# Kernel tuning notes

Measured on AMD Instinct MI355X. Metric: run time of the kernel, lower is better.

## Reference

```python
import jax, jax.numpy as jnp
import numpy as np

P, F_IN, HG, C, T, E, HOUT = 4096, 64, 64, 64, 32, 65536, 12
LEAKY_SLOPE = 0.2
LN_EPS = 1e-5


def setup_inputs() -> dict:
    key = jax.random.key(0)
    ks = jax.random.split(key, 14)
    g = lambda k, shape, scale: (jax.random.normal(k, shape, jnp.float32) * scale)
    return {
        "X": jax.random.normal(ks[0], (1, P, F_IN, T), jnp.float32),
        "edge_index": jax.random.randint(ks[1], (T, 2, E), 0, P, jnp.int32),
        # GATv2 params (single head)
        "Wl": g(ks[2], (F_IN, HG), 0.1),
        "Wr": g(ks[3], (F_IN, HG), 0.1),
        "att": g(ks[4], (HG,), 0.1),
        "gat_b": g(ks[5], (HG,), 0.02),
        # 1x1 time conv (HG -> C) and 1x1 residual conv (F_IN -> C)
        "W_time": g(ks[6], (C, HG), 0.1),
        "b_time": g(ks[7], (C,), 0.02),
        "W_res": g(ks[8], (C, F_IN), 0.1),
        "b_res": g(ks[9], (C,), 0.02),
        # LayerNorm over channel dim C
        "ln_g": jnp.ones((C,), jnp.float32),
        "ln_b": jnp.zeros((C,), jnp.float32),
        # final conv: Conv2d(in=T, out=HOUT, kernel=(1, C)) -> weight (HOUT, T, C)
        "W_final": g(ks[10], (HOUT, T, C), 0.05),
        "b_final": g(ks[11], (HOUT,), 0.02),
    }


def reference(X, edge_index, Wl, Wr, att, gat_b, W_time, b_time, W_res, b_res,
              ln_g, ln_b, W_final, b_final):
    Pn = X.shape[1]

    def gat_t(x, edges):
        # x: (P, F_IN), edges: (2, E) with edges[0]=src j, edges[1]=dst i
        src, dst = edges[0], edges[1]
        hl = x @ Wl                      # (P, HG) messages
        hr = x @ Wr                      # (P, HG) query side
        e = jax.nn.leaky_relu(hl[src] + hr[dst], LEAKY_SLOPE) @ att  # (E,)
        emax = jax.ops.segment_max(e, dst, num_segments=Pn)
        ex = jnp.exp(e - emax[dst])
        den = jax.ops.segment_sum(ex, dst, num_segments=Pn)
        alpha = ex / den[dst]            # softmax over in-edges of each dst
        return jax.ops.segment_sum(alpha[:, None] * hl[src], dst,
                                   num_segments=Pn) + gat_b  # (P, HG)

    xs = jnp.moveaxis(X[0], -1, 0)                     # (T, P, F_IN)
    X_hat = jax.nn.relu(jax.vmap(gat_t)(xs, edge_index))  # (T, P, HG)

    th = jnp.einsum('tph,ch->tpc', X_hat, W_time) + b_time  # time conv 1x1
    rs = jnp.einsum('tpf,cf->tpc', xs, W_res) + b_res       # residual conv 1x1
    y = jax.nn.relu(th + rs)                                 # (T, P, C)

    mu = jnp.mean(y, axis=-1, keepdims=True)
    var = jnp.var(y, axis=-1, keepdims=True)
    yn = (y - mu) * jax.lax.rsqrt(var + LN_EPS) * ln_g + ln_b  # (T, P, C)

    # final conv: in-channels = T, kernel (1, C) -> contract over t and c
    out = jnp.einsum('tpc,otc->po', yn, W_final) + b_final     # (P, HOUT)
    return out[None]                                           # (1, P, HOUT)
```

## Files before the change

kernel.cpp:

```cpp
#include <hip/hip_runtime.h>
#include <math.h>

#define NP 4096
#define F_IN 64
#define HG 64
#define NC 64
#define NT 32
#define NE 65536
#define HOUT 12
#define LEAKY 0.2f
#define LN_EPS 1e-5f

template <int CTRL>
__device__ __forceinline__ float dppadd(float v, float x) {
    int r = __builtin_amdgcn_update_dpp(0, __builtin_bit_cast(int, x), CTRL, 0xF, 0xF, false);
    return v + __builtin_bit_cast(float, r);
}
__device__ __forceinline__ float rowsum16(float v) {
    v = dppadd<0x128>(v, v);
    v = dppadd<0x124>(v, v);
    v = dppadd<0x122>(v, v);
    v = dppadd<0x121>(v, v);
    return v;
}
__device__ __forceinline__ float laneXorSum(float v) {
    v += __shfl_xor(v, 16, 64);
    v += __shfl_xor(v, 32, 64);
    return v;
}
__device__ __forceinline__ int waveSumInt(int v) {
#pragma unroll
    for (int d = 1; d < 64; d <<= 1) v += __shfl_xor(v, d, 64);
    return v;
}

#define FMA4(Acomp, B, r)                                                     \
    acc[r][0] += (Acomp) * (B).x; acc[r][1] += (Acomp) * (B).y;               \
    acc[r][2] += (Acomp) * (B).z; acc[r][3] += (Acomp) * (B).w;

__global__ __launch_bounds__(256) void k_prep(const float* __restrict__ W_time,
        const float* __restrict__ W_res, const float* __restrict__ bf,
        float* __restrict__ wtT, float* __restrict__ wrT, float* __restrict__ out) {
    int b = blockIdx.x, tid = threadIdx.x;
    if (b < 16) {
        int i = b * 256 + tid;
        wtT[i] = W_time[(i & 63) * 64 + (i >> 6)];
    } else if (b < 32) {
        int i = (b - 16) * 256 + tid;
        wrT[i] = W_res[(i & 63) * 64 + (i >> 6)];
    } else {
        int i = (b - 32) * 256 + tid;
        out[i] = bf[i % HOUT];
    }
}

__global__ __launch_bounds__(256) void k_hlhr(const float* __restrict__ X,
        const float* __restrict__ Wl, const float* __restrict__ Wr,
        const float* __restrict__ wrT, const float* __restrict__ b_res,
        float* __restrict__ hl, float* __restrict__ hr, float* __restrict__ rs) {
    __shared__ float xs[2][F_IN][36];
    __shared__ float bk[F_IN][132];
    int p0 = blockIdx.x * 2, tid = threadIdx.x;
    const float4* Xp = (const float4*)(X + (size_t)p0 * F_IN * NT);
    for (int i4 = tid; i4 < 1024; i4 += 256) {
        int pp = i4 >> 9, f = (i4 >> 3) & 63, t0 = (i4 & 7) * 4;
        *(float4*)&xs[pp][f][t0] = Xp[i4];
    }
    const float4* Wl4 = (const float4*)Wl;
    const float4* Wr4 = (const float4*)Wr;
    for (int i4 = tid; i4 < 1024; i4 += 256) {
        int f = i4 >> 4, h4 = (i4 & 15) * 4;
        *(float4*)&bk[f][h4] = Wl4[i4];
        *(float4*)&bk[f][64 + h4] = Wr4[i4];
    }
    __syncthreads();
    {
        int ng = tid & 31, tg = tid >> 5;
        int n0 = ng * 4, col = (ng & 15) * 4, t0 = tg * 4;
        float acc[8][4];
#pragma unroll
        for (int i = 0; i < 8; ++i)
#pragma unroll
            for (int j = 0; j < 4; ++j) acc[i][j] = 0.f;
#pragma unroll 4
        for (int f = 0; f < F_IN; ++f) {
            float4 B = *(const float4*)&bk[f][n0];
            float4 A0 = *(const float4*)&xs[0][f][t0];
            float4 A1 = *(const float4*)&xs[1][f][t0];
            FMA4(A0.x, B, 0) FMA4(A0.y, B, 1) FMA4(A0.z, B, 2) FMA4(A0.w, B, 3)
            FMA4(A1.x, B, 4) FMA4(A1.y, B, 5) FMA4(A1.z, B, 6) FMA4(A1.w, B, 7)
        }
#pragma unroll
        for (int pp = 0; pp < 2; ++pp) {
#pragma unroll
            for (int i = 0; i < 4; ++i) {
                size_t rb = ((size_t)(t0 + i) * NP + p0 + pp) * HG;
                float4 v;
                v.x = acc[pp * 4 + i][0]; v.y = acc[pp * 4 + i][1];
                v.z = acc[pp * 4 + i][2]; v.w = acc[pp * 4 + i][3];
                if (ng < 16) *(float4*)&hl[rb + col] = v;
                else         *(float4*)&hr[rb + col] = v;
            }
        }
    }
    __syncthreads();
    {
        const float4* wrT4 = (const float4*)wrT;
        for (int i4 = tid; i4 < 1024; i4 += 256) {
            int f = i4 >> 4, c4 = (i4 & 15) * 4;
            *(float4*)&bk[f][c4] = wrT4[i4];
        }
    }
    __syncthreads();
    {
        int cg = tid & 15, tg = tid >> 4;
        int c0 = cg * 4, t0 = tg * 2;
        float4 br4 = *(const float4*)&b_res[c0];
        float acc[4][4];
#pragma unroll
        for (int i = 0; i < 4; ++i) {
            acc[i][0] = br4.x; acc[i][1] = br4.y; acc[i][2] = br4.z; acc[i][3] = br4.w;
        }
#pragma unroll 4
        for (int f = 0; f < F_IN; ++f) {
            float4 B = *(const float4*)&bk[f][c0];
            float2 A0 = *(const float2*)&xs[0][f][t0];
            float2 A1 = *(const float2*)&xs[1][f][t0];
            FMA4(A0.x, B, 0) FMA4(A0.y, B, 1)
            FMA4(A1.x, B, 2) FMA4(A1.y, B, 3)
        }
#pragma unroll
        for (int pp = 0; pp < 2; ++pp) {
#pragma unroll
            for (int i = 0; i < 2; ++i) {
                float4 v;
                v.x = acc[pp * 2 + i][0]; v.y = acc[pp * 2 + i][1];
                v.z = acc[pp * 2 + i][2]; v.w = acc[pp * 2 + i][3];
                *(float4*)&rs[((size_t)(t0 + i) * NP + p0 + pp) * NC + c0] = v;
            }
        }
    }
}

__global__ __launch_bounds__(256) void k_count(const int* __restrict__ EI,
        int* __restrict__ cnt2, int* __restrict__ segsum2) {
    __shared__ int loc[1024];
    int b = blockIdx.x;
    int j = b >> 3;
    int t = (b & 7) + 8 * (j & 3);
    int cr = j >> 2;
    int c = cr & 3, r = cr >> 2;
    int tid = threadIdx.x;
    loc[tid] = 0; loc[tid + 256] = 0; loc[tid + 512] = 0; loc[tid + 768] = 0;
    __syncthreads();
    int base = r << 10;
    const int4* dstA = (const int4*)(EI + (size_t)t * 2 * NE + NE) + c * (NE / 16);
    for (int i = tid; i < NE / 16; i += 256) {
        int4 d = dstA[i];
        if ((d.x >> 10) == r) atomicAdd(&loc[d.x - base], 1);
        if ((d.y >> 10) == r) atomicAdd(&loc[d.y - base], 1);
        if ((d.z >> 10) == r) atomicAdd(&loc[d.z - base], 1);
        if ((d.w >> 10) == r) atomicAdd(&loc[d.w - base], 1);
    }
    __syncthreads();
    int o = (t * 4 + c) * NP + base + tid;
    cnt2[o] = loc[tid];
    cnt2[o + 256] = loc[tid + 256];
    cnt2[o + 512] = loc[tid + 512];
    cnt2[o + 768] = loc[tid + 768];
    int wv = tid >> 6, lane = tid & 63;
    int s = loc[wv * 256 + lane] + loc[wv * 256 + lane + 64]
          + loc[wv * 256 + lane + 128] + loc[wv * 256 + lane + 192];
    s = waveSumInt(s);
    if (lane == 0) segsum2[(t * 4 + c) * 16 + r * 4 + wv] = s;
}

__global__ __launch_bounds__(256) void k_scan(const int* __restrict__ cnt2,
        const int* __restrict__ segsum2, int* __restrict__ cnt,
        int* __restrict__ start, int* __restrict__ start2) {
    __shared__ int sc[256];
    __shared__ int preS;
    int b = blockIdx.x;
    int t = b >> 4, seg = b & 15;
    int tid = threadIdx.x;
    if (tid < 64) {
        int c = tid >> 4, s = tid & 15;
        int v = (s < seg) ? segsum2[(t * 4 + c) * 16 + s] : 0;
        v = waveSumInt(v);
        if (tid == 0) preS = v;
    }
    int d = seg * 256 + tid;
    int q0 = cnt2[(t * 4 + 0) * NP + d];
    int q1 = cnt2[(t * 4 + 1) * NP + d];
    int q2 = cnt2[(t * 4 + 2) * NP + d];
    int q3 = cnt2[(t * 4 + 3) * NP + d];
    int deg = q0 + q1 + q2 + q3;
    sc[tid] = deg;
    __syncthreads();
    int pre = preS;
    for (int dd = 1; dd < 256; dd <<= 1) {
        int v = (tid >= dd) ? sc[tid - dd] : 0;
        __syncthreads();
        sc[tid] += v;
        __syncthreads();
    }
    int exc = sc[tid] - deg;
    int st = t * NE + pre + exc;
    cnt[t * NP + d] = deg;
    start[t * NP + d] = st;
    start2[(t * 4 + 0) * NP + d] = st; st += q0;
    start2[(t * 4 + 1) * NP + d] = st; st += q1;
    start2[(t * 4 + 2) * NP + d] = st; st += q2;
    start2[(t * 4 + 3) * NP + d] = st;
}

__global__ __launch_bounds__(256) void k_fill(const int* __restrict__ EI,
        const int* __restrict__ start2, int* __restrict__ ssrc) {
    __shared__ int curs_l[1024];
    int b = blockIdx.x;
    int j = b >> 3;
    int t = (b & 7) + 8 * (j & 3);
    int cr = j >> 2;
    int c = cr & 3, r = cr >> 2;
    int tid = threadIdx.x;
    int base = r << 10;
    int o = (t * 4 + c) * NP + base + tid;
    curs_l[tid] = start2[o];
    curs_l[tid + 256] = start2[o + 256];
    curs_l[tid + 512] = start2[o + 512];
    curs_l[tid + 768] = start2[o + 768];
    __syncthreads();
    const int4* srcA = (const int4*)(EI + (size_t)t * 2 * NE) + c * (NE / 16);
    const int4* dstA = (const int4*)(EI + (size_t)t * 2 * NE + NE) + c * (NE / 16);
    for (int i = tid; i < NE / 16; i += 256) {
        int4 s = srcA[i];
        int4 d = dstA[i];
        if ((d.x >> 10) == r) { int sl = atomicAdd(&curs_l[d.x - base], 1); ssrc[sl] = s.x; }
        if ((d.y >> 10) == r) { int sl = atomicAdd(&curs_l[d.y - base], 1); ssrc[sl] = s.y; }
        if ((d.z >> 10) == r) { int sl = atomicAdd(&curs_l[d.z - base], 1); ssrc[sl] = s.z; }
        if ((d.w >> 10) == r) { int sl = atomicAdd(&curs_l[d.w - base], 1); ssrc[sl] = s.w; }
    }
}

__global__ __launch_bounds__(256) void k_gat(const float* __restrict__ hl,
        float* __restrict__ hr,
        const int* __restrict__ start, const int* __restrict__ cnt,
        const int* __restrict__ ssrc,
        const float* __restrict__ att, const float* __restrict__ gat_b) {
    __shared__ int sidx[4][64];
    int b = blockIdx.x;
    int k = b >> 3;
    int t = (b & 7) + 8 * (k >> 10);
    int ws = threadIdx.x >> 6;
    int i = (k & 1023) * 4 + ws;
    int lane = threadIdx.x & 63;
    int row = lane >> 4;
    int c0 = (lane & 15) * 4;
    size_t nbase = ((size_t)t * NP + i) * HG;
    const float* hlt = hl + (size_t)t * NP * HG;
    float4 r4 = *(const float4*)&hr[nbase + c0];
    float4 at4 = *(const float4*)&att[c0];
    int s0 = start[t * NP + i];
    int deg = cnt[t * NP + i];
    float l = 0.f;
    float4 acc = {0.f, 0.f, 0.f, 0.f};
    for (int base = 0; base < deg; base += 64) {
        int chunk = deg - base;
        chunk = (chunk < 64) ? chunk : 64;
        int stage = (lane < chunk) ? lane : 0;
        sidx[ws][lane] = ssrc[s0 + base + stage];
        int nfull = chunk & ~7;
        int j = 0;
        for (; j < nfull; j += 8) {
            int src0 = sidx[ws][j + row];
            int src1 = sidx[ws][j + 4 + row];
            float4 h0 = *(const float4*)&hlt[((size_t)src0 << 6) + c0];
            float4 h1 = *(const float4*)&hlt[((size_t)src1 << 6) + c0];
            float4 z0, z1;
            z0.x = h0.x + r4.x; z0.y = h0.y + r4.y; z0.z = h0.z + r4.z; z0.w = h0.w + r4.w;
            z1.x = h1.x + r4.x; z1.y = h1.y + r4.y; z1.z = h1.z + r4.z; z1.w = h1.w + r4.w;
            z0.x = fmaxf(z0.x, LEAKY * z0.x); z0.y = fmaxf(z0.y, LEAKY * z0.y);
            z0.z = fmaxf(z0.z, LEAKY * z0.z); z0.w = fmaxf(z0.w, LEAKY * z0.w);
            z1.x = fmaxf(z1.x, LEAKY * z1.x); z1.y = fmaxf(z1.y, LEAKY * z1.y);
            z1.z = fmaxf(z1.z, LEAKY * z1.z); z1.w = fmaxf(z1.w, LEAKY * z1.w);
            float e0 = rowsum16(z0.x * at4.x + z0.y * at4.y + z0.z * at4.z + z0.w * at4.w);
            float e1 = rowsum16(z1.x * at4.x + z1.y * at4.y + z1.z * at4.z + z1.w * at4.w);
            float w0 = __expf(e0);
            float w1 = __expf(e1);
            l += w0 + w1;
            acc.x += w0 * h0.x + w1 * h1.x;
            acc.y += w0 * h0.y + w1 * h1.y;
            acc.z += w0 * h0.z + w1 * h1.z;
            acc.w += w0 * h0.w + w1 * h1.w;
        }
        for (; j < chunk; j += 4) {
            int jj = j + row;
            int src = sidx[ws][(jj < chunk) ? jj : 0];
            float4 ha = *(const float4*)&hlt[((size_t)src << 6) + c0];
            float4 za;
            za.x = ha.x + r4.x; za.y = ha.y + r4.y; za.z = ha.z + r4.z; za.w = ha.w + r4.w;
            za.x = fmaxf(za.x, LEAKY * za.x);
            za.y = fmaxf(za.y, LEAKY * za.y);
            za.z = fmaxf(za.z, LEAKY * za.z);
            za.w = fmaxf(za.w, LEAKY * za.w);
            float ep = za.x * at4.x + za.y * at4.y + za.z * at4.z + za.w * at4.w;
            float e = rowsum16(ep);
            float w = __expf(e);
            w = (jj < chunk) ? w : 0.f;
            l += w;
            acc.x += w * ha.x; acc.y += w * ha.y; acc.z += w * ha.z; acc.w += w * ha.w;
        }
    }
    float lt = laneXorSum(l);
    acc.x = laneXorSum(acc.x);
    acc.y = laneXorSum(acc.y);
    acc.z = laneXorSum(acc.z);
    acc.w = laneXorSum(acc.w);
    if (row == 0) {
        float inv = (deg > 0) ? (1.0f / lt) : 0.f;
        float4 gb = *(const float4*)&gat_b[c0];
        float4 o;
        o.x = fmaxf(acc.x * inv + gb.x, 0.f);
        o.y = fmaxf(acc.y * inv + gb.y, 0.f);
        o.z = fmaxf(acc.z * inv + gb.z, 0.f);
        o.w = fmaxf(acc.w * inv + gb.w, 0.f);
        *(float4*)&hr[nbase + c0] = o;
    }
}

__global__ __launch_bounds__(256) void k_pf(const float* __restrict__ Xhat,
        const float* __restrict__ wtT, const float* __restrict__ b_time,
        const float* __restrict__ rs, const float* __restrict__ ln_g,
        const float* __restrict__ ln_b, const float* __restrict__ Wf,
        float* __restrict__ out) {
    __shared__ float in_t[64][68];
    __shared__ float bk[64][68];
    int bx = blockIdx.x;
    int tc = bx & 7;
    int p0 = (bx >> 3) * 64;
    int tid = threadIdx.x;
    const float4* wsrc = (const float4*)wtT;
    for (int i4 = tid; i4 < 1024; i4 += 256) {
        int h = i4 >> 4, c4 = (i4 & 15) * 4;
        *(float4*)&bk[h][c4] = wsrc[i4];
    }
    int cg = tid & 15, pg = tid >> 4;
    int c0 = cg * 4, pl = pg * 4;
    float4 bt4 = *(const float4*)&b_time[c0];
    float4 lg = *(const float4*)&ln_g[c0];
    float4 lb = *(const float4*)&ln_b[c0];
    float ot[4][HOUT];
#pragma unroll
    for (int i = 0; i < 4; ++i)
#pragma unroll
        for (int o = 0; o < HOUT; ++o) ot[i][o] = 0.f;
    for (int ti = 0; ti < 4; ++ti) {
        int t = tc + ti * 8;
        __syncthreads();
        const float4* src = (const float4*)(Xhat + ((size_t)t * NP + p0) * HG);
        for (int i4 = tid; i4 < 1024; i4 += 256) {
            int pp = i4 >> 4, c4 = (i4 & 15) * 4;
            *(float4*)&in_t[pp][c4] = src[i4];
        }
        __syncthreads();
        float acc[4][4];
#pragma unroll
        for (int i = 0; i < 4; ++i) {
            acc[i][0] = bt4.x; acc[i][1] = bt4.y; acc[i][2] = bt4.z; acc[i][3] = bt4.w;
        }
#pragma unroll
        for (int k4 = 0; k4 < 16; ++k4) {
            float4 A0 = *(const float4*)&in_t[pl + 0][k4 * 4];
            float4 A1 = *(const float4*)&in_t[pl + 1][k4 * 4];
            float4 A2 = *(const float4*)&in_t[pl + 2][k4 * 4];
            float4 A3 = *(const float4*)&in_t[pl + 3][k4 * 4];
            float4 B0 = *(const float4*)&bk[k4 * 4 + 0][c0];
            FMA4(A0.x, B0, 0) FMA4(A1.x, B0, 1) FMA4(A2.x, B0, 2) FMA4(A3.x, B0, 3)
            float4 B1 = *(const float4*)&bk[k4 * 4 + 1][c0];
            FMA4(A0.y, B1, 0) FMA4(A1.y, B1, 1) FMA4(A2.y, B1, 2) FMA4(A3.y, B1, 3)
            float4 B2 = *(const float4*)&bk[k4 * 4 + 2][c0];
            FMA4(A0.z, B2, 0) FMA4(A1.z, B2, 1) FMA4(A2.z, B2, 2) FMA4(A3.z, B2, 3)
            float4 B3 = *(const float4*)&bk[k4 * 4 + 3][c0];
            FMA4(A0.w, B3, 0) FMA4(A1.w, B3, 1) FMA4(A2.w, B3, 2) FMA4(A3.w, B3, 3)
        }
        float4 ynv[4];
#pragma unroll
        for (int i = 0; i < 4; ++i) {
            size_t prow = (size_t)t * NP + p0 + pl + i;
            float4 r4 = *(const float4*)&rs[prow * NC + c0];
            float y0 = fmaxf(acc[i][0] + r4.x, 0.f), y1 = fmaxf(acc[i][1] + r4.y, 0.f);
            float y2 = fmaxf(acc[i][2] + r4.z, 0.f), y3 = fmaxf(acc[i][3] + r4.w, 0.f);
            float s = rowsum16(y0 + y1 + y2 + y3);
            float ss = rowsum16(y0 * y0 + y1 * y1 + y2 * y2 + y3 * y3);
            float mu = s * (1.f / 64.f);
            float var = ss * (1.f / 64.f) - mu * mu;
            float rsd = rsqrtf(var + LN_EPS);
            ynv[i].x = (y0 - mu) * rsd * lg.x + lb.x;
            ynv[i].y = (y1 - mu) * rsd * lg.y + lb.y;
            ynv[i].z = (y2 - mu) * rsd * lg.z + lb.z;
            ynv[i].w = (y3 - mu) * rsd * lg.w + lb.w;
        }
#pragma unroll
        for (int o = 0; o < HOUT; ++o) {
            float4 w4 = *(const float4*)&Wf[(size_t)o * NT * NC + t * NC + c0];
#pragma unroll
            for (int i = 0; i < 4; ++i)
                ot[i][o] += ynv[i].x * w4.x + ynv[i].y * w4.y
                          + ynv[i].z * w4.z + ynv[i].w * w4.w;
        }
    }
#pragma unroll
    for (int i = 0; i < 4; ++i)
#pragma unroll
        for (int o = 0; o < HOUT; ++o) ot[i][o] = rowsum16(ot[i][o]);
    if (cg == 0) {
#pragma unroll
        for (int i = 0; i < 4; ++i) {
            int p = p0 + pl + i;
#pragma unroll
            for (int o = 0; o < HOUT; ++o)
                atomicAdd(&out[p * HOUT + o], ot[i][o]);
        }
    }
}

extern "C" void kernel_launch(void* const* d_in, const int* in_sizes, int n_in,
                              void* d_out, int out_size, void* d_ws, size_t ws_size,
                              hipStream_t stream) {
    const float* X      = (const float*)d_in[0];
    const int*   EI     = (const int*)d_in[1];
    const float* Wl     = (const float*)d_in[2];
    const float* Wr     = (const float*)d_in[3];
    const float* att    = (const float*)d_in[4];
    const float* gat_b  = (const float*)d_in[5];
    const float* W_time = (const float*)d_in[6];
    const float* b_time = (const float*)d_in[7];
    const float* W_res  = (const float*)d_in[8];
    const float* b_res  = (const float*)d_in[9];
    const float* ln_g   = (const float*)d_in[10];
    const float* ln_b   = (const float*)d_in[11];
    const float* Wf     = (const float*)d_in[12];
    const float* bf     = (const float*)d_in[13];
    float* out = (float*)d_out;

    char* ws = (char*)d_ws;
    const size_t MB = 1024 * 1024;
    float* hl    = (float*)(ws);
    float* hr    = (float*)(ws + 32 * MB);
    float* rs    = (float*)(ws + 64 * MB);
    int*   ssrc  = (int*)  (ws + 96 * MB);
    int*   cnt   = (int*)  (ws + 104 * MB);
    int*   strt  = (int*)  (ws + 104 * MB + 512 * 1024);
    float* wtT   = (float*)(ws + 105 * MB);
    float* wrT   = (float*)(ws + 105 * MB + 16384);
    int*   segs2 = (int*)  (ws + 105 * MB + 32768);
    int*   cnt2  = (int*)  (ws + 106 * MB);
    int*   strt2 = (int*)  (ws + 108 * MB);

    k_prep <<<224, 256, 0, stream>>>(W_time, W_res, bf, wtT, wrT, out);
    k_hlhr <<<NP / 2, 256, 0, stream>>>(X, Wl, Wr, wrT, b_res, hl, hr, rs);
    k_count<<<512, 256, 0, stream>>>(EI, cnt2, segs2);
    k_scan <<<NT * 16, 256, 0, stream>>>(cnt2, segs2, cnt, strt, strt2);
    k_fill <<<512, 256, 0, stream>>>(EI, strt2, ssrc);
    k_gat  <<<(NT * NP) / 4, 256, 0, stream>>>(hl, hr, strt, cnt, ssrc, att, gat_b);
    k_pf   <<<512, 256, 0, stream>>>(hr, wtT, b_time, rs, ln_g, ln_b, Wf, out);
}
```

Measured before the change: 286.3 us.

## Merge prep, projection and edge-count kernels into one front kernel

Combines k_prep, k_hlhr and k_count into a single launch, with block ranges dispatched to edge counting, node projections, W_time transpose and output bias init. This lets the memory-bound counting overlap with the projection GEMM and removes two launches. Edge chunking goes from 4 to 8 per timestep, doubling count/fill block counts for more parallelism at the cost of scanning 8 partial counts. k_scan now writes the per-chunk start offsets back into cnt2 in place, and W_res is transposed directly into shared memory instead of through a separate wrT buffer.

Result: faster. 279.0 us (-2.5%).

```diff
diff --git a/kernel.cpp b/kernel.cpp
--- a/kernel.cpp
+++ b/kernel.cpp
@@ -38,163 +38,160 @@
     acc[r][0] += (Acomp) * (B).x; acc[r][1] += (Acomp) * (B).y;               \
     acc[r][2] += (Acomp) * (B).z; acc[r][3] += (Acomp) * (B).w;
 
-__global__ __launch_bounds__(256) void k_prep(const float* __restrict__ W_time,
-        const float* __restrict__ W_res, const float* __restrict__ bf,
-        float* __restrict__ wtT, float* __restrict__ wrT, float* __restrict__ out) {
-    int b = blockIdx.x, tid = threadIdx.x;
-    if (b < 16) {
-        int i = b * 256 + tid;
+__global__ __launch_bounds__(256) void k_front(const float* __restrict__ X,
+        const float* __restrict__ Wl, const float* __restrict__ Wr,
+        const float* __restrict__ W_res, const float* __restrict__ b_res,
+        const float* __restrict__ W_time, const float* __restrict__ bf,
+        const int* __restrict__ EI,
+        float* __restrict__ hl, float* __restrict__ hr, float* __restrict__ rs,
+        float* __restrict__ wtT, float* __restrict__ out,
+        int* __restrict__ cnt2, int* __restrict__ segsum2) {
+    __shared__ float smem[13312];
+    int b = blockIdx.x;
+    int tid = threadIdx.x;
+    if (b < 1024) {
+        int* loc = (int*)smem;
+        int j = b >> 3;
+        int t = (b & 7) + 8 * (j & 3);
+        int cr = j >> 2;
+        int c = cr & 7, r = cr >> 3;
+        loc[tid] = 0; loc[tid + 256] = 0; loc[tid + 512] = 0; loc[tid + 768] = 0;
+        __syncthreads();
+        int base = r << 10;
+        const int4* dstA = (const int4*)(EI + (size_t)t * 2 * NE + NE) + c * (NE / 32);
+        for (int i = tid; i < NE / 32; i += 256) {
+            int4 d = dstA[i];
+            if ((d.x >> 10) == r) atomicAdd(&loc[d.x - base], 1);
+            if ((d.y >> 10) == r) atomicAdd(&loc[d.y - base], 1);
+            if ((d.z >> 10) == r) atomicAdd(&loc[d.z - base], 1);
+            if ((d.w >> 10) == r) atomicAdd(&loc[d.w - base], 1);
+        }
+        __syncthreads();
+        int o = (t * 8 + c) * NP + base + tid;
+        cnt2[o] = loc[tid];
+        cnt2[o + 256] = loc[tid + 256];
+        cnt2[o + 512] = loc[tid + 512];
+        cnt2[o + 768] = loc[tid + 768];
+        int wv = tid >> 6, lane = tid & 63;
+        int s = loc[wv * 256 + lane] + loc[wv * 256 + lane + 64]
+              + loc[wv * 256 + lane + 128] + loc[wv * 256 + lane + 192];
+        s = waveSumInt(s);
+        if (lane == 0) segsum2[(t * 8 + c) * 16 + r * 4 + wv] = s;
+    } else if (b < 3072) {
+        float (*xs)[F_IN][36] = (float (*)[F_IN][36])smem;
+        float (*bk)[132] = (float (*)[132])(smem + 4608);
+        int p0 = (b - 1024) * 2;
+        const float4* Xp = (const float4*)(X + (size_t)p0 * F_IN * NT);
+        for (int i4 = tid; i4 < 1024; i4 += 256) {
+            int pp = i4 >> 9, f = (i4 >> 3) & 63, t0 = (i4 & 7) * 4;
+            *(float4*)&xs[pp][f][t0] = Xp[i4];
+        }
+        const float4* Wl4 = (const float4*)Wl;
+        const float4* Wr4 = (const float4*)Wr;
+        for (int i4 = tid; i4 < 1024; i4 += 256) {
+            int f = i4 >> 4, h4 = (i4 & 15) * 4;
+            *(float4*)&bk[f][h4] = Wl4[i4];
+            *(float4*)&bk[f][64 + h4] = Wr4[i4];
+        }
+        __syncthreads();
+        {
+            int ng = tid & 31, tg = tid >> 5;
+            int n0 = ng * 4, col = (ng & 15) * 4, t0 = tg * 4;
+            float acc[8][4];
+#pragma unroll
+            for (int i = 0; i < 8; ++i)
+#pragma unroll
+                for (int j2 = 0; j2 < 4; ++j2) acc[i][j2] = 0.f;
+#pragma unroll 4
+            for (int f = 0; f < F_IN; ++f) {
+                float4 B = *(const float4*)&bk[f][n0];
+                float4 A0 = *(const float4*)&xs[0][f][t0];
+                float4 A1 = *(const float4*)&xs[1][f][t0];
+                FMA4(A0.x, B, 0) FMA4(A0.y, B, 1) FMA4(A0.z, B, 2) FMA4(A0.w, B, 3)
+                FMA4(A1.x, B, 4) FMA4(A1.y, B, 5) FMA4(A1.z, B, 6) FMA4(A1.w, B, 7)
+            }
+#pragma unroll
+            for (int pp = 0; pp < 2; ++pp) {
+#pragma unroll
+                for (int i = 0; i < 4; ++i) {
+                    size_t rb = ((size_t)(t0 + i) * NP + p0 + pp) * HG;
+                    float4 v;
+                    v.x = acc[pp * 4 + i][0]; v.y = acc[pp * 4 + i][1];
+                    v.z = acc[pp * 4 + i][2]; v.w = acc[pp * 4 + i][3];
+                    if (ng < 16) *(float4*)&hl[rb + col] = v;
+                    else         *(float4*)&hr[rb + col] = v;
+                }
+            }
+        }
+        __syncthreads();
+        for (int i = tid; i < F_IN * NC; i += 256) {
+            int c = i >> 6, f = i & 63;
+            bk[f][c] = W_res[i];
+        }
+        __syncthreads();
+        {
+            int cg = tid & 15, tg = tid >> 4;
+            int c0 = cg * 4, t0 = tg * 2;
+            float4 br4 = *(const float4*)&b_res[c0];
+            float acc[4][4];
+#pragma unroll
+            for (int i = 0; i < 4; ++i) {
+                acc[i][0] = br4.x; acc[i][1] = br4.y; acc[i][2] = br4.z; acc[i][3] = br4.w;
+            }
+#pragma unroll 4
+            for (int f = 0; f < F_IN; ++f) {
+                float4 B = *(const float4*)&bk[f][c0];
+                float2 A0 = *(const float2*)&xs[0][f][t0];
+                float2 A1 = *(const float2*)&xs[1][f][t0];
+                FMA4(A0.x, B, 0) FMA4(A0.y, B, 1)
+                FMA4(A1.x, B, 2) FMA4(A1.y, B, 3)
+            }
+#pragma unroll
+            for (int pp = 0; pp < 2; ++pp) {
+#pragma unroll
+                for (int i = 0; i < 2; ++i) {
+                    float4 v;
+                    v.x = acc[pp * 2 + i][0]; v.y = acc[pp * 2 + i][1];
+                    v.z = acc[pp * 2 + i][2]; v.w = acc[pp * 2 + i][3];
+                    *(float4*)&rs[((size_t)(t0 + i) * NP + p0 + pp) * NC + c0] = v;
+                }
+            }
+        }
+    } else if (b < 3088) {
+        int i = (b - 3072) * 256 + tid;
         wtT[i] = W_time[(i & 63) * 64 + (i >> 6)];
-    } else if (b < 32) {
-        int i = (b - 16) * 256 + tid;
-        wrT[i] = W_res[(i & 63) * 64 + (i >> 6)];
     } else {
-        int i = (b - 32) * 256 + tid;
+        int i = (b - 3088) * 256 + tid;
         out[i] = bf[i % HOUT];
     }
 }
 
-__global__ __launch_bounds__(256) void k_hlhr(const float* __restrict__ X,
-        const float* __restrict__ Wl, const float* __restrict__ Wr,
-        const float* __restrict__ wrT, const float* __restrict__ b_res,
-        float* __restrict__ hl, float* __restrict__ hr, float* __restrict__ rs) {
-    __shared__ float xs[2][F_IN][36];
-    __shared__ float bk[F_IN][132];
-    int p0 = blockIdx.x * 2, tid = threadIdx.x;
-    const float4* Xp = (const float4*)(X + (size_t)p0 * F_IN * NT);
-    for (int i4 = tid; i4 < 1024; i4 += 256) {
-        int pp = i4 >> 9, f = (i4 >> 3) & 63, t0 = (i4 & 7) * 4;
-        *(float4*)&xs[pp][f][t0] = Xp[i4];
-    }
-    const float4* Wl4 = (const float4*)Wl;
-    const float4* Wr4 = (const float4*)Wr;
-    for (int i4 = tid; i4 < 1024; i4 += 256) {
-        int f = i4 >> 4, h4 = (i4 & 15) * 4;
-        *(float4*)&bk[f][h4] = Wl4[i4];
-        *(float4*)&bk[f][64 + h4] = Wr4[i4];
-    }
-    __syncthreads();
-    {
-        int ng = tid & 31, tg = tid >> 5;
-        int n0 = ng * 4, col = (ng & 15) * 4, t0 = tg * 4;
-        float acc[8][4];
-#pragma unroll
-        for (int i = 0; i < 8; ++i)
-#pragma unroll
-            for (int j = 0; j < 4; ++j) acc[i][j] = 0.f;
-#pragma unroll 4
-        for (int f = 0; f < F_IN; ++f) {
-            float4 B = *(const float4*)&bk[f][n0];
-            float4 A0 = *(const float4*)&xs[0][f][t0];
-            float4 A1 = *(const float4*)&xs[1][f][t0];
-            FMA4(A0.x, B, 0) FMA4(A0.y, B, 1) FMA4(A0.z, B, 2) FMA4(A0.w, B, 3)
-            FMA4(A1.x, B, 4) FMA4(A1.y, B, 5) FMA4(A1.z, B, 6) FMA4(A1.w, B, 7)
-        }
-#pragma unroll
-        for (int pp = 0; pp < 2; ++pp) {
-#pragma unroll
-            for (int i = 0; i < 4; ++i) {
-                size_t rb = ((size_t)(t0 + i) * NP + p0 + pp) * HG;
-                float4 v;
-                v.x = acc[pp * 4 + i][0]; v.y = acc[pp * 4 + i][1];
-                v.z = acc[pp * 4 + i][2]; v.w = acc[pp * 4 + i][3];
-                if (ng < 16) *(float4*)&hl[rb + col] = v;
-                else         *(float4*)&hr[rb + col] = v;
-            }
-        }
-    }
-    __syncthreads();
-    {
-        const float4* wrT4 = (const float4*)wrT;
-        for (int i4 = tid; i4 < 1024; i4 += 256) {
-            int f = i4 >> 4, c4 = (i4 & 15) * 4;
-            *(float4*)&bk[f][c4] = wrT4[i4];
-        }
-    }
-    __syncthreads();
-    {
-        int cg = tid & 15, tg = tid >> 4;
-        int c0 = cg * 4, t0 = tg * 2;
-        float4 br4 = *(const float4*)&b_res[c0];
-        float acc[4][4];
-#pragma unroll
-        for (int i = 0; i < 4; ++i) {
-            acc[i][0] = br4.x; acc[i][1] = br4.y; acc[i][2] = br4.z; acc[i][3] = br4.w;
-        }
-#pragma unroll 4
-        for (int f = 0; f < F_IN; ++f) {
-            float4 B = *(const float4*)&bk[f][c0];
-            float2 A0 = *(const float2*)&xs[0][f][t0];
-            float2 A1 = *(const float2*)&xs[1][f][t0];
-            FMA4(A0.x, B, 0) FMA4(A0.y, B, 1)
-            FMA4(A1.x, B, 2) FMA4(A1.y, B, 3)
-        }
-#pragma unroll
-        for (int pp = 0; pp < 2; ++pp) {
-#pragma unroll
-            for (int i = 0; i < 2; ++i) {
-                float4 v;
-                v.x = acc[pp * 2 + i][0]; v.y = acc[pp * 2 + i][1];
-                v.z = acc[pp * 2 + i][2]; v.w = acc[pp * 2 + i][3];
-                *(float4*)&rs[((size_t)(t0 + i) * NP + p0 + pp) * NC + c0] = v;
-            }
-        }
-    }
-}
-
-__global__ __launch_bounds__(256) void k_count(const int* __restrict__ EI,
-        int* __restrict__ cnt2, int* __restrict__ segsum2) {
-    __shared__ int loc[1024];
-    int b = blockIdx.x;
-    int j = b >> 3;
-    int t = (b & 7) + 8 * (j & 3);
-    int cr = j >> 2;
-    int c = cr & 3, r = cr >> 2;
-    int tid = threadIdx.x;
-    loc[tid] = 0; loc[tid + 256] = 0; loc[tid + 512] = 0; loc[tid + 768] = 0;
-    __syncthreads();
-    int base = r << 10;
-    const int4* dstA = (const int4*)(EI + (size_t)t * 2 * NE + NE) + c * (NE / 16);
-    for (int i = tid; i < NE / 16; i += 256) {
-        int4 d = dstA[i];
-        if ((d.x >> 10) == r) atomicAdd(&loc[d.x - base], 1);
-        if ((d.y >> 10) == r) atomicAdd(&loc[d.y - base], 1);
-        if ((d.z >> 10) == r) atomicAdd(&loc[d.z - base], 1);
-        if ((d.w >> 10) == r) atomicAdd(&loc[d.w - base], 1);
-    }
-    __syncthreads();
-    int o = (t * 4 + c) * NP + base + tid;
-    cnt2[o] = loc[tid];
-    cnt2[o + 256] = loc[tid + 256];
-    cnt2[o + 512] = loc[tid + 512];
-    cnt2[o + 768] = loc[tid + 768];
-    int wv = tid >> 6, lane = tid & 63;
-    int s = loc[wv * 256 + lane] + loc[wv * 256 + lane + 64]
-          + loc[wv * 256 + lane + 128] + loc[wv * 256 + lane + 192];
-    s = waveSumInt(s);
-    if (lane == 0) segsum2[(t * 4 + c) * 16 + r * 4 + wv] = s;
-}
-
-__global__ __launch_bounds__(256) void k_scan(const int* __restrict__ cnt2,
+__global__ __launch_bounds__(256) void k_scan(int* __restrict__ cnt2,
         const int* __restrict__ segsum2, int* __restrict__ cnt,
-        int* __restrict__ start, int* __restrict__ start2) {
+        int* __restrict__ start) {
     __shared__ int sc[256];
     __shared__ int preS;
     int b = blockIdx.x;
     int t = b >> 4, seg = b & 15;
     int tid = threadIdx.x;
     if (tid < 64) {
-        int c = tid >> 4, s = tid & 15;
-        int v = (s < seg) ? segsum2[(t * 4 + c) * 16 + s] : 0;
+        int s = tid & 15, cp = tid >> 4;
+        int v = 0;
+        if (s < seg) {
+            v = segsum2[(t * 8 + cp * 2 + 0) * 16 + s]
+              + segsum2[(t * 8 + cp * 2 + 1) * 16 + s];
+        }
         v = waveSumInt(v);
         if (tid == 0) preS = v;
     }
     int d = seg * 256 + tid;
-    int q0 = cnt2[(t * 4 + 0) * NP + d];
-    int q1 = cnt2[(t * 4 + 1) * NP + d];
-    int q2 = cnt2[(t * 4 + 2) * NP + d];
-    int q3 = cnt2[(t * 4 + 3) * NP + d];
-    int deg = q0 + q1 + q2 + q3;
+    int q[8];
+    int deg = 0;
+#pragma unroll
+    for (int c = 0; c < 8; ++c) {
+        q[c] = cnt2[(t * 8 + c) * NP + d];
+        deg += q[c];
+    }
     sc[tid] = deg;
     __syncthreads();
     int pre = preS;
@@ -208,10 +205,12 @@
     int st = t * NE + pre + exc;
     cnt[t * NP + d] = deg;
     start[t * NP + d] = st;
-    start2[(t * 4 + 0) * NP + d] = st; st += q0;
-    start2[(t * 4 + 1) * NP + d] = st; st += q1;
-    start2[(t * 4 + 2) * NP + d] = st; st += q2;
-    start2[(t * 4 + 3) * NP + d] = st;
+#pragma unroll
+    for (int c = 0; c < 8; ++c) {
+        int qq = q[c];
+        cnt2[(t * 8 + c) * NP + d] = st;
+        st += qq;
+    }
 }
 
 __global__ __launch_bounds__(256) void k_fill(const int* __restrict__ EI,
@@ -221,18 +220,18 @@
     int j = b >> 3;
     int t = (b & 7) + 8 * (j & 3);
     int cr = j >> 2;
-    int c = cr & 3, r = cr >> 2;
+    int c = cr & 7, r = cr >> 3;
     int tid = threadIdx.x;
     int base = r << 10;
-    int o = (t * 4 + c) * NP + base + tid;
+    int o = (t * 8 + c) * NP + base + tid;
     curs_l[tid] = start2[o];
     curs_l[tid + 256] = start2[o + 256];
     curs_l[tid + 512] = start2[o + 512];
     curs_l[tid + 768] = start2[o + 768];
     __syncthreads();
-    const int4* srcA = (const int4*)(EI + (size_t)t * 2 * NE) + c * (NE / 16);
-    const int4* dstA = (const int4*)(EI + (size_t)t * 2 * NE + NE) + c * (NE / 16);
-    for (int i = tid; i < NE / 16; i += 256) {
+    const int4* srcA = (const int4*)(EI + (size_t)t * 2 * NE) + c * (NE / 32);
+    const int4* dstA = (const int4*)(EI + (size_t)t * 2 * NE + NE) + c * (NE / 32);
+    for (int i = tid; i < NE / 32; i += 256) {
         int4 s = srcA[i];
         int4 d = dstA[i];
         if ((d.x >> 10) == r) { int sl = atomicAdd(&curs_l[d.x - base], 1); ssrc[sl] = s.x; }
@@ -452,16 +451,13 @@
     int*   cnt   = (int*)  (ws + 104 * MB);
     int*   strt  = (int*)  (ws + 104 * MB + 512 * 1024);
     float* wtT   = (float*)(ws + 105 * MB);
-    float* wrT   = (float*)(ws + 105 * MB + 16384);
     int*   segs2 = (int*)  (ws + 105 * MB + 32768);
     int*   cnt2  = (int*)  (ws + 106 * MB);
-    int*   strt2 = (int*)  (ws + 108 * MB);
-
-    k_prep <<<224, 256, 0, stream>>>(W_time, W_res, bf, wtT, wrT, out);
-    k_hlhr <<<NP / 2, 256, 0, stream>>>(X, Wl, Wr, wrT, b_res, hl, hr, rs);
-    k_count<<<512, 256, 0, stream>>>(EI, cnt2, segs2);
-    k_scan <<<NT * 16, 256, 0, stream>>>(cnt2, segs2, cnt, strt, strt2);
-    k_fill <<<512, 256, 0, stream>>>(EI, strt2, ssrc);
+
+    k_front<<<3280, 256, 0, stream>>>(X, Wl, Wr, W_res, b_res, W_time, bf, EI,
+                                      hl, hr, rs, wtT, out, cnt2, segs2);
+    k_scan <<<NT * 16, 256, 0, stream>>>(cnt2, segs2, cnt, strt);
+    k_fill <<<1024, 256, 0, stream>>>(EI, cnt2, ssrc);
     k_gat  <<<(NT * NP) / 4, 256, 0, stream>>>(hl, hr, strt, cnt, ssrc, att, gat_b);
     k_pf   <<<512, 256, 0, stream>>>(hr, wtT, b_time, rs, ln_g, ln_b, Wf, out);
 }
```
